# Kernel optimization log

Hardware: AMD Instinct MI355X
Metric: run time of the kernel (lower is better)

The kernel has to match this reference:

```python
import jax, jax.numpy as jnp
import numpy as np

N = 1026     # tickers (hardcoded in original module)
T = 8        # price window length; self.T = T-1 = 7
H = 64       # hidden dim
F_IN = 5     # price features
E = 1026     # number of hyperedges
NNZ = 200000 # incidence entries per hypergraph


def leaky(x):
    return jnp.where(x >= 0, x, 0.2 * x)


def gru_fwd(x, Wih, Whh, bih, bhh):
    # torch.nn.GRU, batch_first. x: [N, T, F_IN] -> full [N,T,H], last [N,H]
    def step(h, xt):
        gi = xt @ Wih.T + bih
        gh = h @ Whh.T + bhh
        ir, iz, inn = jnp.split(gi, 3, axis=-1)
        hr, hz, hn = jnp.split(gh, 3, axis=-1)
        r = jax.nn.sigmoid(ir + hr)
        z = jax.nn.sigmoid(iz + hz)
        n = jnp.tanh(inn + r * hn)
        h = (1.0 - z) * n + z * h
        return h, h
    h0 = jnp.zeros((x.shape[0], H), x.dtype)
    last, full = jax.lax.scan(step, h0, jnp.swapaxes(x, 0, 1))
    return jnp.swapaxes(full, 0, 1), last


def hyp_conv(x, idx, theta, bias):
    # PyG HypergraphConv (use_attention=False): out = D^-1 H B^-1 H^T (X theta) + bias
    node, edge = idx[0], idx[1]
    ones = jnp.ones(node.shape, x.dtype)
    deg_n = jax.ops.segment_sum(ones, node, num_segments=N)
    deg_e = jax.ops.segment_sum(ones, edge, num_segments=E)
    Dinv = jnp.where(deg_n > 0, 1.0 / deg_n, 0.0)
    Binv = jnp.where(deg_e > 0, 1.0 / deg_e, 0.0)
    xt = x @ theta
    e = jax.ops.segment_sum(xt[node] * Binv[edge][:, None], edge, num_segments=E)
    out = jax.ops.segment_sum(e[edge], node, num_segments=N) * Dinv[:, None]
    return out + bias


def decayed_attention(query, context, Win, Wout, ae, ab):
    # query [N,1,H], context [N,T,H]; 'general' attention with temporal-decay term
    q = jnp.einsum('nod,de->noe', query, Win)
    w = jax.nn.softmax(jnp.einsum('nod,ntd->not', q, context), axis=-1)  # [N,1,T]
    mix = w * jnp.swapaxes(context, 1, 2)                                # [N,H,T]
    delta = jnp.arange(T - 1, -1, -1, dtype=context.dtype).reshape(1, 1, T)
    bt = jnp.exp(-ab * delta)                                            # [N,1,T]
    term2 = jax.nn.relu(ae * mix * bt)
    mixs = jnp.sum(term2 + mix, axis=-1)[:, None, :]                     # [N,1,H]
    comb = jnp.concatenate([mixs, q], axis=2).reshape(N, 2 * H)
    return jnp.tanh(comb @ Wout).reshape(N, H), w


def _forward(price_input, hyp_T, hyp, Wih, Whh, bih, bhh, Win, Wout, ae, ab,
             theta1, bias1, theta2, bias2, w1, w2, a_param, Wl, bl):
    context, last = gru_fwd(price_input, Wih, Whh, bih, bhh)
    output, _ = decayed_attention(last[:, None, :], context, Win, Wout, ae, ab)  # [N,H]

    def per_t(idx):
        x1 = leaky(hyp_conv(output, idx, theta1, bias1))
        return leaky(hyp_conv(x1, idx, theta2, bias2))

    x2 = jax.vmap(per_t)(hyp_T)            # [T, N, H]
    sub = x2[1:] - x2[:-1]                 # diff(): [T-1, N, H]
    b = jnp.mean(sub, axis=(1, 2), keepdims=True)
    U = 1.0 / (1.0 + a_param * (b - sub))  # c = 1
    z = ((U * sub) / U).sum(axis=(1, 2))   # [T-1] (faithful to original)
    wattn = jax.nn.softmax(w2 @ leaky(w1 @ z), axis=0)  # [T-1]
    concat = wattn[:, None, None] * sub
    xx1 = concat[0] + concat[2]            # stack([0],[2]) then sum over dim 0
    xg = leaky(hyp_conv(output, hyp, theta1, bias1))
    xg = leaky(hyp_conv(xg, hyp, theta2, bias2))
    oput = jnp.concatenate([xg, xx1], axis=1)  # [N, 2H]
    return leaky(oput @ Wl + bl)               # [N, 1]


def setup_inputs() -> dict:
    key = jax.random.key(0)
    ks = jax.random.split(key, 24)
    def xn(k, shape, scale=None):
        fan = (shape[-2] + shape[-1]) if len(shape) >= 2 else shape[0]
        s = scale if scale is not None else float(np.sqrt(2.0 / fan))
        return jax.random.normal(k, shape, dtype=jnp.float32) * s
    inp = {}
    inp['price_input'] = jax.random.normal(ks[0], (N, T, F_IN), dtype=jnp.float32)
    node_T = jax.random.randint(ks[1], (T, 1, NNZ), 0, N)
    edge_T = jax.random.randint(ks[2], (T, 1, NNZ), 0, E)
    inp['hyp_T'] = jnp.concatenate([node_T, edge_T], axis=1).astype(jnp.int32)
    node = jax.random.randint(ks[3], (1, NNZ), 0, N)
    edge = jax.random.randint(ks[4], (1, NNZ), 0, E)
    inp['hyp'] = jnp.concatenate([node, edge], axis=0).astype(jnp.int32)
    inp['Wih'] = xn(ks[5], (3 * H, F_IN))
    inp['Whh'] = xn(ks[6], (3 * H, H))
    std = float(1.0 / np.sqrt(3 * H))
    inp['bih'] = jax.random.uniform(ks[7], (3 * H,), minval=-std, maxval=std, dtype=jnp.float32)
    inp['bhh'] = jax.random.uniform(ks[8], (3 * H,), minval=-std, maxval=std, dtype=jnp.float32)
    inp['Win'] = xn(ks[9], (H, H))
    inp['Wout'] = xn(ks[10], (2 * H, H))
    inp['ae'] = xn(ks[11], (N, 1, 1), scale=0.05)
    inp['ab'] = jnp.abs(xn(ks[12], (N, 1, 1), scale=0.05))
    inp['theta1'] = xn(ks[13], (H, H))
    inp['bias1'] = jax.random.uniform(ks[14], (H,), minval=-0.125, maxval=0.125, dtype=jnp.float32)
    inp['theta2'] = xn(ks[15], (H, H))
    inp['bias2'] = jax.random.uniform(ks[16], (H,), minval=-0.125, maxval=0.125, dtype=jnp.float32)
    inp['w1'] = xn(ks[17], (H, T - 1))
    inp['w2'] = xn(ks[18], (T - 1, H))
    inp['a_param'] = xn(ks[19], (T - 1, 1, 1), scale=0.05)
    inp['Wl'] = xn(ks[20], (2 * H, 1))
    inp['bl'] = jax.random.uniform(ks[21], (1,), minval=-0.088, maxval=0.088, dtype=jnp.float32)
    return inp


def reference(price_input, hyp_T, hyp, Wih, Whh, bih, bhh, Win, Wout, ae, ab,
              theta1, bias1, theta2, bias2, w1, w2, a_param, Wl, bl):
    return _forward(price_input, hyp_T, hyp, Wih, Whh, bih, bhh, Win, Wout, ae, ab,
                    theta1, bias1, theta2, bias2, w1, w2, a_param, Wl, bl)
```

## Files before the change

kernel.cpp:

```cpp
#include <hip/hip_runtime.h>
#include <hip/hip_bf16.h>
#include <math.h>

#define N 1026
#define T 8
#define H 64
#define F_IN 5
#define E 1026
#define NNZ 200000
#define TM 7
#define NG 9
#define KP 1056
#define NWB 132
#define RT 96
#define NT 11
#define NH (N*H)
#define WT 193
#define BZC 32
#define CHUNK (NH/BZC)

#define OFF_PRICE   0
#define OFF_WIH     41040
#define OFF_WHH     42000
#define OFF_BIH     54288
#define OFF_BHH     54480
#define OFF_WIN     54672
#define OFF_WOUT    58768
#define OFF_AE      66960
#define OFF_AB      67986
#define OFF_TH1     69012
#define OFF_B1      73108
#define OFF_TH2     73172
#define OFF_B2      77268
#define OFF_W1      77332
#define OFF_W2      77780
#define OFF_APAR    78228
#define OFF_WL      78235
#define OFF_BL      78363
#define TOT_CVT     78364

typedef unsigned int u32;
typedef unsigned short u16;
typedef short bf16x8 __attribute__((ext_vector_type(8)));
typedef float f32x4 __attribute__((ext_vector_type(4)));

__device__ __forceinline__ float leakyf(float x){ return x >= 0.f ? x : 0.2f*x; }
__device__ __forceinline__ float bfbits2f(u16 u){
  union { u32 i; float f; } c; c.i = ((u32)u) << 16; return c.f;
}
__device__ __forceinline__ u16 f2bf(float f){
  u32 x = __builtin_bit_cast(u32, f);
  u32 r = x + 0x7FFFu + ((x >> 16) & 1u);
  return (u16)(r >> 16);
}
__device__ __forceinline__ int detect_f32(const u16* __restrict__ w){
  int lane = threadIdx.x & 63;
  int big = 0;
  for (int k = lane; k < 960; k += 64){
    float a = fabsf(bfbits2f(w[k]));
    if (!(a < 1e3f)) big = 1;
  }
  return (__ballot(big != 0) != 0ull) ? 1 : 0;
}

struct CvtPtrs { const void* p[18]; };

__global__ __launch_bounds__(256) void k_cvt(CvtPtrs ps, float* __restrict__ dst){
  const int offs[19] = {OFF_PRICE, OFF_WIH, OFF_WHH, OFF_BIH, OFF_BHH, OFF_WIN,
                        OFF_WOUT, OFF_AE, OFF_AB, OFF_TH1, OFF_B1, OFF_TH2,
                        OFF_B2, OFF_W1, OFF_W2, OFF_APAR, OFF_WL, OFF_BL, TOT_CVT};
  int isf32 = detect_f32((const u16*)ps.p[1]);
  int i = blockIdx.x*256 + threadIdx.x;
  if (i < TOT_CVT){
    int t = 0;
    #pragma unroll
    for (int k = 1; k < 18; k++) if (i >= offs[k]) t = k;
    int j = i - offs[t];
    float v;
    if (isf32) v = ((const float*)ps.p[t])[j];
    else       v = bfbits2f(((const u16*)ps.p[t])[j]);
    dst[i] = v;
  }
}

__global__ __launch_bounds__(1024) void k_build(const int* __restrict__ hypT,
                                                const int* __restrict__ hyp,
                                                u16* __restrict__ AHm,
                                                u16* __restrict__ AHmT,
                                                float* __restrict__ Dinv,
                                                float* __restrict__ Binv){
  __shared__ u32 bins[RT*NWB];
  int tid = threadIdx.x;
  int g = blockIdx.y, side = blockIdx.z;
  int r0 = blockIdx.x * RT;
  for (int k = tid; k < RT*NWB; k += 1024) bins[k] = 0;
  __syncthreads();
  const int4* np4; const int4* ep4;
  if (g < 8){ const int* np_ = hypT + (size_t)g*2*NNZ;
              np4 = (const int4*)np_; ep4 = (const int4*)(np_ + NNZ); }
  else      { np4 = (const int4*)hyp; ep4 = (const int4*)(hyp + NNZ); }
  #pragma unroll 4
  for (int i = tid; i < NNZ/4; i += 1024){
    int4 a4 = np4[i], b4 = ep4[i];
    int ra[4], ca[4];
    if (side){
      ra[0]=b4.x; ra[1]=b4.y; ra[2]=b4.z; ra[3]=b4.w;
      ca[0]=a4.x; ca[1]=a4.y; ca[2]=a4.z; ca[3]=a4.w;
    } else {
      ra[0]=a4.x; ra[1]=a4.y; ra[2]=a4.z; ra[3]=a4.w;
      ca[0]=b4.x; ca[1]=b4.y; ca[2]=b4.z; ca[3]=b4.w;
    }
    #pragma unroll
    for (int e = 0; e < 4; e++){
      int rr = ra[e] - r0;
      if ((unsigned)rr < (unsigned)RT)
        atomicAdd(&bins[rr*NWB + (ca[e]>>3)], 1u << ((ca[e]&7)*4));
    }
  }
  __syncthreads();
  {
    int r = tid >> 3, j = tid & 7;
    if (r < RT){
      u32 s = 0;
      for (int w = j; w < NWB; w += 8){
        u32 v = bins[r*NWB + w];
        u32 a = (v & 0x0F0F0F0Fu) + ((v >> 4) & 0x0F0F0F0Fu);
        s += (a * 0x01010101u) >> 24;
      }
      s += __shfl_xor(s, 1); s += __shfl_xor(s, 2); s += __shfl_xor(s, 4);
      int gr = r0 + r;
      if (j == 0 && gr < N){
        float inv = s ? 1.f/(float)s : 0.f;
        (side ? Binv : Dinv)[g*N + gr] = inv;
      }
    }
  }
  u16* dst = (side ? AHmT : AHm) + (size_t)g*KP*KP;
  for (int idx = tid; idx < RT*NWB; idx += 1024){
    int rr = idx / NWB, w = idx - rr*NWB;
    u32 v = bins[rr*NWB + w];
    bf16x8 o;
    #pragma unroll
    for (int j = 0; j < 8; j++)
      o[j] = (short)f2bf((float)((v >> (4*j)) & 0xFu));
    *(bf16x8*)(dst + (size_t)(r0 + rr)*KP + w*8) = o;
  }
}

__global__ __launch_bounds__(256) void k_gruattn(const float* __restrict__ price,
                                                 const float* __restrict__ Wih,
                                                 const float* __restrict__ Whh,
                                                 const float* __restrict__ bih,
                                                 const float* __restrict__ bhh,
                                                 const float* __restrict__ Win,
                                                 const float* __restrict__ Wout,
                                                 const float* __restrict__ ae,
                                                 const float* __restrict__ ab,
                                                 float* __restrict__ outp){
  __shared__ __align__(16) char smem[64640];
  float* sc  = (float*)smem;
  float* shh = (float*)(smem + 8192);
  char* ph = smem + 9216;
  float* sWhhT = (float*)ph;
  float* sWih  = (float*)(ph + 49408);
  float* sbih  = (float*)(ph + 53248);
  float* sbhh  = (float*)(ph + 54016);
  float* sx    = (float*)(ph + 54784);
  int tid = threadIdx.x, w = tid>>6, lane = tid&63;
  int n = blockIdx.x*4 + w;
  for (int idx = tid; idx < 192*64; idx += 256){
    int j = idx >> 6, d = idx & 63;
    sWhhT[d*WT + j] = Whh[idx];
  }
  for (int k = tid; k < 192*F_IN; k += 256) sWih[k] = Wih[k];
  for (int k = tid; k < 192;      k += 256){ sbih[k] = bih[k]; sbhh[k] = bhh[k]; }
  if (n < N){ for (int k = lane; k < T*F_IN; k += 64) sx[w*40 + k] = price[(size_t)n*T*F_IN + k]; }
  else      { for (int k = lane; k < T*F_IN; k += 64) sx[w*40 + k] = 0.f; }
  shh[w*64 + lane] = 0.f;
  __syncthreads();
  for (int t = 0; t < T; t++){
    float ir = sbih[lane], iz = sbih[64+lane], inn = sbih[128+lane];
    #pragma unroll
    for (int d = 0; d < F_IN; d++){
      float x = sx[w*40 + t*F_IN + d];
      ir  += x * sWih[lane*F_IN + d];
      iz  += x * sWih[(64+lane)*F_IN + d];
      inn += x * sWih[(128+lane)*F_IN + d];
    }
    float hr = sbhh[lane], hz = sbhh[64+lane], hn = sbhh[128+lane];
    for (int d = 0; d < 64; d++){
      float hv = shh[w*64 + d];
      const float* wr = &sWhhT[d*WT];
      hr += hv * wr[lane];
      hz += hv * wr[64 + lane];
      hn += hv * wr[128 + lane];
    }
    float r  = 1.f/(1.f + expf(-(ir+hr)));
    float z  = 1.f/(1.f + expf(-(iz+hz)));
    float nn = tanhf(inn + r*hn);
    float hnew = (1.f - z)*nn + z*shh[w*64 + lane];
    __syncthreads();
    shh[w*64 + lane] = hnew;
    sc[w*512 + t*64 + lane] = hnew;
    __syncthreads();
  }
  float* sWin  = (float*)ph;
  float* sWout = (float*)(ph + 16384);
  float* sq    = (float*)(ph + 49152);
  float* ssv   = (float*)(ph + 50176);
  float* sco   = (float*)(ph + 50304);
  for (int k = tid; k < 1024; k += 256) ((float4*)sWin)[k]  = ((const float4*)Win)[k];
  for (int k = tid; k < 2048; k += 256) ((float4*)sWout)[k] = ((const float4*)Wout)[k];
  __syncthreads();
  float q = 0.f;
  for (int d = 0; d < 64; d++) q += shh[w*64 + d]*sWin[d*64 + lane];
  sq[w*64 + lane] = q;
  __syncthreads();
  if (lane < T){
    float s = 0.f;
    for (int d = 0; d < 64; d++) s += sq[w*64 + d]*sc[w*512 + lane*64 + d];
    ssv[w*8 + lane] = s;
  }
  __syncthreads();
  float m = ssv[w*8 + 0];
  for (int t = 1; t < T; t++) m = fmaxf(m, ssv[w*8 + t]);
  float wv[T]; float den = 0.f;
  for (int t = 0; t < T; t++){ wv[t] = expf(ssv[w*8 + t]-m); den += wv[t]; }
  float aen = (n < N) ? ae[n] : 0.f, abn = (n < N) ? ab[n] : 0.f;
  float mixs = 0.f;
  for (int t = 0; t < T; t++){
    float wt = wv[t]/den;
    float mx = wt * sc[w*512 + t*64 + lane];
    float bt = expf(-abn * (float)(T-1-t));
    mixs += fmaxf(aen*mx*bt, 0.f) + mx;
  }
  sco[w*128 + lane] = mixs; sco[w*128 + 64 + lane] = q;
  __syncthreads();
  float o = 0.f;
  for (int k = 0; k < 128; k++) o += sco[w*128 + k]*sWout[k*64 + lane];
  if (n < N) outp[(size_t)n*H + lane] = tanhf(o);
}

__global__ __launch_bounds__(256) void k_xthetaT(const float* __restrict__ x,
                                                 const float* __restrict__ theta,
                                                 int x_per_graph,
                                                 u16* __restrict__ xtT){
  __shared__ float sth[4096];
  __shared__ float sxr[64][64];
  __shared__ float syt[64][65];
  int tid = threadIdx.x, w = tid>>6, lane = tid&63;
  int g = blockIdx.y;
  int r0 = blockIdx.x*64;
  const float* xg = x + (x_per_graph ? (size_t)g*N*64 : (size_t)0);
  for (int k = tid; k < 1024; k += 256) ((float4*)sth)[k] = ((const float4*)theta)[k];
  for (int rr = w; rr < 64; rr += 4){
    int r = r0 + rr;
    sxr[rr][lane] = (r < N) ? xg[(size_t)r*64 + lane] : 0.f;
  }
  __syncthreads();
  for (int rr = w*16; rr < w*16+16; rr++){
    float acc = 0.f;
    for (int d = 0; d < 64; d++) acc = fmaf(sxr[rr][d], sth[d*64 + lane], acc);
    syt[lane][rr] = acc;
  }
  __syncthreads();
  int col = r0 + lane;
  if (col < KP){
    for (int f = w*16; f < w*16+16; f++)
      xtT[((size_t)g*64 + f)*KP + col] = f2bf(syt[f][lane]);
  }
}

__global__ __launch_bounds__(64) void k_gemm(const u16* __restrict__ A,
                                             const u16* __restrict__ Xt,
                                             int x_per_graph,
                                             const float* __restrict__ scale,
                                             const float* __restrict__ bias,
                                             int mode,
                                             u16* __restrict__ Yt,
                                             float* __restrict__ Yf){
  int g = blockIdx.y;
  int m0 = (blockIdx.x >> 2) * 16;
  int nt = blockIdx.x & 3;
  int lane = threadIdx.x;
  int mrow = lane & 15, quad = lane >> 4;
  const u16* Ap = A + (size_t)g*KP*KP + (size_t)(m0 + mrow)*KP + quad*8;
  const u16* Bp = Xt + (x_per_graph ? (size_t)g*64*KP : (size_t)0)
                     + (size_t)(nt*16 + mrow)*KP + quad*8;
  f32x4 acc = (f32x4){0.f,0.f,0.f,0.f};
  bf16x8 a0 = *(const bf16x8*)Ap;
  bf16x8 b0 = *(const bf16x8*)Bp;
  for (int c = 0; c < 33; c++){
    bf16x8 a1 = a0, b1 = b0;
    if (c < 32){
      a1 = *(const bf16x8*)(Ap + (c+1)*32);
      b1 = *(const bf16x8*)(Bp + (c+1)*32);
    }
    acc = __builtin_amdgcn_mfma_f32_16x16x32_bf16(a0, b0, acc, 0, 0, 0);
    a0 = a1; b0 = b1;
  }
  int mbase = m0 + quad*4;
  float sc_[4];
  #pragma unroll
  for (int r = 0; r < 4; r++){
    int m = mbase + r;
    sc_[r] = (m < N) ? scale[g*N + m] : 0.f;
  }
  if (mode == 0){
    ushort4 o;
    o.x = f2bf(acc[0]*sc_[0]);
    o.y = f2bf(acc[1]*sc_[1]);
    o.z = f2bf(acc[2]*sc_[2]);
    o.w = f2bf(acc[3]*sc_[3]);
    *(ushort4*)(Yt + ((size_t)g*64 + nt*16 + mrow)*KP + mbase) = o;
  } else {
    float bs = bias[nt*16 + mrow];
    #pragma unroll
    for (int r = 0; r < 4; r++){
      int m = mbase + r;
      if (m < N){
        float v = acc[r]*sc_[r] + bs;
        Yf[((size_t)g*N + m)*64 + nt*16 + mrow] = leakyf(v);
      }
    }
  }
}

__global__ __launch_bounds__(256) void k_bz1(const float* __restrict__ x2,
                                             float* __restrict__ bpart){
  int k = blockIdx.x, ch = blockIdx.y, tid = threadIdx.x;
  int wv = tid >> 6, lane = tid & 63;
  const float4* a4 = (const float4*)(x2 + (size_t)k*NH + (size_t)ch*CHUNK);
  const float4* c4 = (const float4*)(x2 + (size_t)(k+1)*NH + (size_t)ch*CHUNK);
  float s = 0.f;
  for (int i = tid; i < CHUNK/4; i += 256){
    float4 cc = c4[i], aa = a4[i];
    s += (cc.x-aa.x)+(cc.y-aa.y)+(cc.z-aa.z)+(cc.w-aa.w);
  }
  __shared__ float red[4];
  for (int off = 32; off; off >>= 1) s += __shfl_down(s, off);
  if (lane == 0) red[wv] = s;
  __syncthreads();
  if (tid == 0) bpart[k*BZC + ch] = red[0]+red[1]+red[2]+red[3];
}

__global__ __launch_bounds__(256) void k_bz2(const float* __restrict__ x2,
                                             const float* __restrict__ bpart,
                                             const float* __restrict__ a_param,
                                             float* __restrict__ zpart){
  int k = blockIdx.x, ch = blockIdx.y, tid = threadIdx.x;
  int wv = tid >> 6, lane = tid & 63;
  __shared__ float sbk;
  if (tid == 0){
    float t = 0.f;
    for (int j = 0; j < BZC; j++) t += bpart[k*BZC + j];
    sbk = t / (float)NH;
  }
  __syncthreads();
  float bk = sbk, ap = a_param[k];
  const float4* a4 = (const float4*)(x2 + (size_t)k*NH + (size_t)ch*CHUNK);
  const float4* c4 = (const float4*)(x2 + (size_t)(k+1)*NH + (size_t)ch*CHUNK);
  float s = 0.f;
  for (int i = tid; i < CHUNK/4; i += 256){
    float4 cc = c4[i], aa = a4[i];
    float sb[4] = {cc.x-aa.x, cc.y-aa.y, cc.z-aa.z, cc.w-aa.w};
    #pragma unroll
    for (int j = 0; j < 4; j++){
      float U = 1.f/(1.f + ap*(bk - sb[j]));
      s += (U*sb[j])/U;
    }
  }
  __shared__ float red[4];
  for (int off = 32; off; off >>= 1) s += __shfl_down(s, off);
  if (lane == 0) red[wv] = s;
  __syncthreads();
  if (tid == 0) zpart[k*BZC + ch] = red[0]+red[1]+red[2]+red[3];
}

__global__ __launch_bounds__(256) void k_final(const float* __restrict__ x2,
                                               const float* __restrict__ zpart,
                                               const float* __restrict__ w1,
                                               const float* __restrict__ w2,
                                               const float* __restrict__ Wl,
                                               const float* __restrict__ bl,
                                               const u16* __restrict__ wihRaw,
                                               void* __restrict__ outv){
  __shared__ float sz[8];
  __shared__ float sy[64];
  __shared__ float swa[8];
  int tid = threadIdx.x;
  int isf32 = detect_f32(wihRaw);
  if (tid < TM){
    float t = 0.f;
    for (int j = 0; j < BZC; j++) t += zpart[tid*BZC + j];
    sz[tid] = t;
  }
  __syncthreads();
  if (tid < 64){
    float y = 0.f;
    for (int kk = 0; kk < TM; kk++) y += w1[tid*TM + kk]*sz[kk];
    sy[tid] = leakyf(y);
  }
  __syncthreads();
  if (tid < TM){
    float v = 0.f;
    for (int d = 0; d < 64; d++) v += w2[tid*64 + d]*sy[d];
    swa[tid] = v;
  }
  __syncthreads();
  if (tid == 0){
    float m = swa[0];
    for (int t = 1; t < TM; t++) m = fmaxf(m, swa[t]);
    float den = 0.f;
    for (int t = 0; t < TM; t++){ swa[t] = expf(swa[t]-m); den += swa[t]; }
    for (int t = 0; t < TM; t++) swa[t] /= den;
  }
  __syncthreads();
  int n = blockIdx.x*256 + tid;
  if (n < N){
    float w0 = swa[0], w2v = swa[2];
    float acc = bl[0];
    for (int h = 0; h < 64; h++){
      float xg = x2[(size_t)8*NH + (size_t)n*64 + h];
      float s0 = x2[(size_t)1*NH + (size_t)n*64 + h] - x2[(size_t)0*NH + (size_t)n*64 + h];
      float s2 = x2[(size_t)3*NH + (size_t)n*64 + h] - x2[(size_t)2*NH + (size_t)n*64 + h];
      float xx = w0*s0 + w2v*s2;
      acc += xg*Wl[h] + xx*Wl[64 + h];
    }
    float r = leakyf(acc);
    if (isf32) ((float*)outv)[n] = r;
    else       ((__hip_bfloat16*)outv)[n] = __float2bfloat16(r);
  }
}

extern "C" void kernel_launch(void* const* d_in, const int* in_sizes, int n_in,
                              void* d_out, int out_size, void* d_ws, size_t ws_size,
                              hipStream_t stream) {
  const int* hypT = (const int*)d_in[1];
  const int* hyp  = (const int*)d_in[2];

  char* p = (char*)d_ws;
  auto alloc = [&](size_t bytes) -> char* {
    char* r = p; p += (bytes + 63) & ~(size_t)63; return r;
  };
  float* cv   = (float*)alloc((size_t)TOT_CVT*4);
  u16* AHm    = (u16*)  alloc((size_t)NG*KP*KP*2);
  u16* AHmT   = (u16*)  alloc((size_t)NG*KP*KP*2);
  float* Dinv = (float*)alloc((size_t)NG*N*4);
  float* Binv = (float*)alloc((size_t)NG*N*4);
  float* outp = (float*)alloc((size_t)N*H*4);
  float* x1   = (float*)alloc((size_t)NG*N*H*4);
  float* x2   = (float*)alloc((size_t)NG*N*H*4);
  float* bpart= (float*)alloc((size_t)TM*BZC*4);
  float* zpart= (float*)alloc((size_t)TM*BZC*4);
  u16* xtT1   = (u16*)  alloc((size_t)64*KP*2);
  u16* xtT2   = (u16*)  alloc((size_t)NG*64*KP*2);
  u16* ebufT  = (u16*)  alloc((size_t)NG*64*KP*2);

  const float* price  = cv + OFF_PRICE;
  const float* Wih    = cv + OFF_WIH;
  const float* Whh    = cv + OFF_WHH;
  const float* bih    = cv + OFF_BIH;
  const float* bhh    = cv + OFF_BHH;
  const float* Win    = cv + OFF_WIN;
  const float* Wout   = cv + OFF_WOUT;
  const float* ae     = cv + OFF_AE;
  const float* ab     = cv + OFF_AB;
  const float* theta1 = cv + OFF_TH1;
  const float* bias1  = cv + OFF_B1;
  const float* theta2 = cv + OFF_TH2;
  const float* bias2  = cv + OFF_B2;
  const float* w1     = cv + OFF_W1;
  const float* w2     = cv + OFF_W2;
  const float* a_par  = cv + OFF_APAR;
  const float* Wl     = cv + OFF_WL;
  const float* bl     = cv + OFF_BL;

  CvtPtrs ps;
  ps.p[0]=d_in[0];  ps.p[1]=d_in[3];  ps.p[2]=d_in[4];  ps.p[3]=d_in[5];
  ps.p[4]=d_in[6];  ps.p[5]=d_in[7];  ps.p[6]=d_in[8];  ps.p[7]=d_in[9];
  ps.p[8]=d_in[10]; ps.p[9]=d_in[11]; ps.p[10]=d_in[12]; ps.p[11]=d_in[13];
  ps.p[12]=d_in[14]; ps.p[13]=d_in[15]; ps.p[14]=d_in[16]; ps.p[15]=d_in[17];
  ps.p[16]=d_in[18]; ps.p[17]=d_in[19];
  k_cvt<<<(TOT_CVT+255)/256, 256, 0, stream>>>(ps, cv);

  k_build<<<dim3(NT, NG, 2), 1024, 0, stream>>>(hypT, hyp, AHm, AHmT, Dinv, Binv);
  k_gruattn<<<(N+3)/4, 256, 0, stream>>>(price, Wih, Whh, bih, bhh,
                                         Win, Wout, ae, ab, outp);

  k_xthetaT<<<dim3(17, 1), 256, 0, stream>>>(outp, theta1, 0, xtT1);
  k_gemm<<<dim3((KP/16)*4, NG), 64, 0, stream>>>(AHmT, xtT1, 0, Binv, nullptr, 0, ebufT, nullptr);
  k_gemm<<<dim3((KP/16)*4, NG), 64, 0, stream>>>(AHm, ebufT, 1, Dinv, bias1, 1, nullptr, x1);

  k_xthetaT<<<dim3(17, NG), 256, 0, stream>>>(x1, theta2, 1, xtT2);
  k_gemm<<<dim3((KP/16)*4, NG), 64, 0, stream>>>(AHmT, xtT2, 1, Binv, nullptr, 0, ebufT, nullptr);
  k_gemm<<<dim3((KP/16)*4, NG), 64, 0, stream>>>(AHm, ebufT, 1, Dinv, bias2, 1, nullptr, x2);

  k_bz1<<<dim3(TM, BZC), 256, 0, stream>>>(x2, bpart);
  k_bz2<<<dim3(TM, BZC), 256, 0, stream>>>(x2, bpart, a_par, zpart);
  k_final<<<(N+255)/256, 256, 0, stream>>>(x2, zpart, w1, w2, Wl, bl,
                                           (const u16*)d_in[3], d_out);
}
```

Baseline: 299.4 us.

## Restructure GRU-attention kernel to one node per block with register-held weights

The GRU+attention kernel now assigns one node per 256-thread block instead of four nodes (one per wave). The 48KB transposed Whh staging in shared memory is replaced by each wave holding a 16-column slice of Whh in registers, with partial sums reduced through shared memory. The input projection is precomputed for all timesteps up front, and the Win/Wout matvecs are split across waves. This removes the large per-block shared-memory load and raises occupancy, at the cost of four times more blocks, repeated global weight reads per block, and extra barriers per timestep.

```diff
diff --git a/kernel.cpp b/kernel.cpp
--- a/kernel.cpp
+++ b/kernel.cpp
@@ -15,7 +15,6 @@
 #define RT 96
 #define NT 11
 #define NH (N*H)
-#define WT 193
 #define BZC 32
 #define CHUNK (NH/BZC)
 
@@ -157,88 +156,106 @@
                                                  const float* __restrict__ ae,
                                                  const float* __restrict__ ab,
                                                  float* __restrict__ outp){
-  __shared__ __align__(16) char smem[64640];
-  float* sc  = (float*)smem;
-  float* shh = (float*)(smem + 8192);
-  char* ph = smem + 9216;
-  float* sWhhT = (float*)ph;
-  float* sWih  = (float*)(ph + 49408);
-  float* sbih  = (float*)(ph + 53248);
-  float* sbhh  = (float*)(ph + 54016);
-  float* sx    = (float*)(ph + 54784);
+  __shared__ float gi[T][192];
+  __shared__ float sh[64];
+  __shared__ float sctx[T*64];
+  __shared__ float part[4][192];
+  __shared__ float sx[T*F_IN];
+  __shared__ float sq[64];
+  __shared__ float ssc[T];
+  __shared__ float sco[128];
   int tid = threadIdx.x, w = tid>>6, lane = tid&63;
-  int n = blockIdx.x*4 + w;
-  for (int idx = tid; idx < 192*64; idx += 256){
-    int j = idx >> 6, d = idx & 63;
-    sWhhT[d*WT + j] = Whh[idx];
-  }
-  for (int k = tid; k < 192*F_IN; k += 256) sWih[k] = Wih[k];
-  for (int k = tid; k < 192;      k += 256){ sbih[k] = bih[k]; sbhh[k] = bhh[k]; }
-  if (n < N){ for (int k = lane; k < T*F_IN; k += 64) sx[w*40 + k] = price[(size_t)n*T*F_IN + k]; }
-  else      { for (int k = lane; k < T*F_IN; k += 64) sx[w*40 + k] = 0.f; }
-  shh[w*64 + lane] = 0.f;
+  int n = blockIdx.x;
+  float wr_[16], wz_[16], wn_[16];
+  #pragma unroll
+  for (int j = 0; j < 16; j++){
+    int d = w*16 + j;
+    wr_[j] = Whh[(size_t)(      lane)*64 + d];
+    wz_[j] = Whh[(size_t)( 64 + lane)*64 + d];
+    wn_[j] = Whh[(size_t)(128 + lane)*64 + d];
+  }
+  if (tid < T*F_IN) sx[tid] = price[(size_t)n*T*F_IN + tid];
+  if (tid < 64) sh[tid] = 0.f;
+  __syncthreads();
+  for (int idx = tid; idx < T*192; idx += 256){
+    int t = idx / 192, gd = idx - t*192;
+    float acc = bih[gd];
+    #pragma unroll
+    for (int d5 = 0; d5 < F_IN; d5++)
+      acc = fmaf(sx[t*F_IN + d5], Wih[gd*F_IN + d5], acc);
+    gi[t][gd] = acc;
+  }
   __syncthreads();
   for (int t = 0; t < T; t++){
-    float ir = sbih[lane], iz = sbih[64+lane], inn = sbih[128+lane];
-    #pragma unroll
-    for (int d = 0; d < F_IN; d++){
-      float x = sx[w*40 + t*F_IN + d];
-      ir  += x * sWih[lane*F_IN + d];
-      iz  += x * sWih[(64+lane)*F_IN + d];
-      inn += x * sWih[(128+lane)*F_IN + d];
-    }
-    float hr = sbhh[lane], hz = sbhh[64+lane], hn = sbhh[128+lane];
-    for (int d = 0; d < 64; d++){
-      float hv = shh[w*64 + d];
-      const float* wr = &sWhhT[d*WT];
-      hr += hv * wr[lane];
-      hz += hv * wr[64 + lane];
-      hn += hv * wr[128 + lane];
-    }
-    float r  = 1.f/(1.f + expf(-(ir+hr)));
-    float z  = 1.f/(1.f + expf(-(iz+hz)));
-    float nn = tanhf(inn + r*hn);
-    float hnew = (1.f - z)*nn + z*shh[w*64 + lane];
+    float pr = 0.f, pz = 0.f, pn = 0.f;
+    #pragma unroll
+    for (int j = 0; j < 16; j++){
+      float hv = sh[w*16 + j];
+      pr = fmaf(hv, wr_[j], pr);
+      pz = fmaf(hv, wz_[j], pz);
+      pn = fmaf(hv, wn_[j], pn);
+    }
+    part[w][lane] = pr; part[w][64 + lane] = pz; part[w][128 + lane] = pn;
     __syncthreads();
-    shh[w*64 + lane] = hnew;
-    sc[w*512 + t*64 + lane] = hnew;
+    if (tid < 64){
+      int o = tid;
+      float hr = bhh[o]       + part[0][o]     + part[1][o]     + part[2][o]     + part[3][o];
+      float hz = bhh[64 + o]  + part[0][64+o]  + part[1][64+o]  + part[2][64+o]  + part[3][64+o];
+      float hn = bhh[128 + o] + part[0][128+o] + part[1][128+o] + part[2][128+o] + part[3][128+o];
+      float r  = 1.f/(1.f + expf(-(gi[t][o] + hr)));
+      float z  = 1.f/(1.f + expf(-(gi[t][64 + o] + hz)));
+      float nn = tanhf(gi[t][128 + o] + r*hn);
+      float hnew = (1.f - z)*nn + z*sh[o];
+      sh[o] = hnew;
+      sctx[t*64 + o] = hnew;
+    }
     __syncthreads();
   }
-  float* sWin  = (float*)ph;
-  float* sWout = (float*)(ph + 16384);
-  float* sq    = (float*)(ph + 49152);
-  float* ssv   = (float*)(ph + 50176);
-  float* sco   = (float*)(ph + 50304);
-  for (int k = tid; k < 1024; k += 256) ((float4*)sWin)[k]  = ((const float4*)Win)[k];
-  for (int k = tid; k < 2048; k += 256) ((float4*)sWout)[k] = ((const float4*)Wout)[k];
-  __syncthreads();
-  float q = 0.f;
-  for (int d = 0; d < 64; d++) q += shh[w*64 + d]*sWin[d*64 + lane];
-  sq[w*64 + lane] = q;
-  __syncthreads();
-  if (lane < T){
+  {
+    float qp = 0.f;
+    #pragma unroll
+    for (int j = 0; j < 16; j++)
+      qp = fmaf(sh[w*16 + j], Win[(size_t)(w*16 + j)*64 + lane], qp);
+    part[w][lane] = qp;
+  }
+  __syncthreads();
+  if (tid < 64) sq[tid] = part[0][tid] + part[1][tid] + part[2][tid] + part[3][tid];
+  __syncthreads();
+  if (tid < T){
     float s = 0.f;
-    for (int d = 0; d < 64; d++) s += sq[w*64 + d]*sc[w*512 + lane*64 + d];
-    ssv[w*8 + lane] = s;
-  }
-  __syncthreads();
-  float m = ssv[w*8 + 0];
-  for (int t = 1; t < T; t++) m = fmaxf(m, ssv[w*8 + t]);
-  float wv[T]; float den = 0.f;
-  for (int t = 0; t < T; t++){ wv[t] = expf(ssv[w*8 + t]-m); den += wv[t]; }
-  float aen = (n < N) ? ae[n] : 0.f, abn = (n < N) ? ab[n] : 0.f;
-  float mixs = 0.f;
-  for (int t = 0; t < T; t++){
-    float wt = wv[t]/den;
-    float mx = wt * sc[w*512 + t*64 + lane];
-    float bt = expf(-abn * (float)(T-1-t));
-    mixs += fmaxf(aen*mx*bt, 0.f) + mx;
-  }
-  sco[w*128 + lane] = mixs; sco[w*128 + 64 + lane] = q;
-  __syncthreads();
-  float o = 0.f;
-  for (int k = 0; k < 128; k++) o += sco[w*128 + k]*sWout[k*64 + lane];
-  if (n < N) outp[(size_t)n*H + lane] = tanhf(o);
+    for (int d = 0; d < 64; d++) s = fmaf(sq[d], sctx[tid*64 + d], s);
+    ssc[tid] = s;
+  }
+  __syncthreads();
+  if (tid < 64){
+    int o = tid;
+    float m = ssc[0];
+    for (int t = 1; t < T; t++) m = fmaxf(m, ssc[t]);
+    float wv[T]; float den = 0.f;
+    for (int t = 0; t < T; t++){ wv[t] = expf(ssc[t] - m); den += wv[t]; }
+    float aen = ae[n], abn = ab[n];
+    float mixs = 0.f;
+    for (int t = 0; t < T; t++){
+      float wt = wv[t]/den;
+      float mx = wt * sctx[t*64 + o];
+      float bt = expf(-abn * (float)(T-1-t));
+      mixs += fmaxf(aen*mx*bt, 0.f) + mx;
+    }
+    sco[o] = mixs; sco[64 + o] = sq[o];
+  }
+  __syncthreads();
+  {
+    float op = 0.f;
+    #pragma unroll
+    for (int j = 0; j < 32; j++)
+      op = fmaf(sco[w*32 + j], Wout[(size_t)(w*32 + j)*64 + lane], op);
+    part[w][lane] = op;
+  }
+  __syncthreads();
+  if (tid < 64){
+    float o = part[0][tid] + part[1][tid] + part[2][tid] + part[3][tid];
+    outp[(size_t)n*H + tid] = tanhf(o);
+  }
 }
 
 __global__ __launch_bounds__(256) void k_xthetaT(const float* __restrict__ x,
@@ -485,8 +502,8 @@
   k_cvt<<<(TOT_CVT+255)/256, 256, 0, stream>>>(ps, cv);
 
   k_build<<<dim3(NT, NG, 2), 1024, 0, stream>>>(hypT, hyp, AHm, AHmT, Dinv, Binv);
-  k_gruattn<<<(N+3)/4, 256, 0, stream>>>(price, Wih, Whh, bih, bhh,
-                                         Win, Wout, ae, ab, outp);
+  k_gruattn<<<N, 256, 0, stream>>>(price, Wih, Whh, bih, bhh,
+                                   Win, Wout, ae, ab, outp);
 
   k_xthetaT<<<dim3(17, 1), 256, 0, stream>>>(outp, theta1, 0, xtT1);
   k_gemm<<<dim3((KP/16)*4, NG), 64, 0, stream>>>(AHmT, xtT1, 0, Binv, nullptr, 0, ebufT, nullptr);
```

New measurement: 271.7 us (median of 3 runs). 1.1x faster.
